# Kernel optimization log

Measured on AMD Instinct MI355X. Metric: run time of the kernel, lower is better.

The kernel has to match this reference:

```python
import jax, jax.numpy as jnp
import numpy as np

INPUT_DIM = 256
UNITS = 256
BATCH = 65536


def _glorot(key, shape):
    fan_in, fan_out = shape
    limit = np.sqrt(6.0 / (fan_in + fan_out)).astype(np.float32)
    return jax.random.uniform(key, shape, jnp.float32, -limit, limit)


def setup_inputs() -> dict:
    key = jax.random.key(0)
    ks = jax.random.split(key, 8)
    d = {
        "inputs": jax.random.normal(ks[0], (BATCH, INPUT_DIM), jnp.float32),
        "h_prev": jax.random.normal(ks[1], (BATCH, UNITS), jnp.float32),
        "c_prev": jax.random.normal(ks[2], (BATCH, UNITS), jnp.float32),
        "W_f": _glorot(ks[3], (INPUT_DIM + UNITS, UNITS)),
        "W_i": _glorot(ks[4], (INPUT_DIM + UNITS, UNITS)),
        "W_c": _glorot(ks[5], (INPUT_DIM + UNITS, UNITS)),
        "W_o": _glorot(ks[6], (INPUT_DIM + UNITS, UNITS)),
        "b_f": jnp.zeros((UNITS,), jnp.float32),
        "b_i": jnp.zeros((UNITS,), jnp.float32),
        "b_c": jnp.zeros((UNITS,), jnp.float32),
        "b_o": jnp.zeros((UNITS,), jnp.float32),
    }
    return d


def reference(inputs, h_prev, c_prev, W_f, W_i, W_c, W_o, b_f, b_i, b_c, b_o):
    # z: [B, input_dim + units]
    z = jnp.concatenate([inputs, h_prev], axis=-1)
    f = jax.nn.sigmoid(z @ W_f + b_f)
    i = jax.nn.sigmoid(z @ W_i + b_i)
    c_tilde = jnp.tanh(z @ W_c + b_c)
    c = f * c_prev + i * c_tilde
    o = jax.nn.sigmoid(z @ W_o + b_o)
    h = o * jnp.tanh(c)
    return h, c
```

## Files before the change

kernel.cpp:

```cpp
#include <hip/hip_runtime.h>
#include <stdint.h>

#define BATCH   65536
#define UNITS   256
#define KDIM    512
#define BM      64
#define BN      64
#define NCHUNK  8
#define GPAD    72
#define SMEM_BYTES 36864

using f32x16 = __attribute__((ext_vector_type(16))) float;
using bf16x8 = __attribute__((ext_vector_type(8))) short;

__device__ __forceinline__ short f2bf(float f) {
  union { float f; unsigned u; } v; v.f = f;
  unsigned r = v.u + 0x7FFFu + ((v.u >> 16) & 1u);
  return (short)(r >> 16);
}
__device__ __forceinline__ float bf2f(short s) {
  union { float f; unsigned u; } v; v.u = ((unsigned)(unsigned short)s) << 16;
  return v.f;
}

__global__ void cvt_weights(const float* __restrict__ Wf, const float* __restrict__ Wi,
                            const float* __restrict__ Wc, const float* __restrict__ Wo,
                            short* __restrict__ Wt) {
  int idx = blockIdx.x * 256 + threadIdx.x;
  int g   = idx >> 17;
  int k   = (idx >> 8) & 511;
  int col = idx & 255;
  const float* W = (g == 0) ? Wf : (g == 1) ? Wi : (g == 2) ? Wc : Wo;
  float val = W[k * 256 + col];
  int nb = col >> 6, n = col & 63;
  int c = k >> 6, kg = (k >> 3) & 7, k8 = k & 7;
  int out = ((((g * 4 + nb) * 8 + c) * 8 + kg) * 64 + n) * 8 + k8;
  Wt[out] = f2bf(val);
}

__global__ __launch_bounds__(256, 3) void lstm_fused(
    const float* __restrict__ x, const float* __restrict__ hprev,
    const float* __restrict__ cprev, const short* __restrict__ Wt,
    const float* __restrict__ bfp, const float* __restrict__ bip,
    const float* __restrict__ bcp, const float* __restrict__ bop,
    float* __restrict__ hout, float* __restrict__ cout)
{
  extern __shared__ __align__(16) char smem[];
  const int tid  = threadIdx.x;
  const int g    = tid >> 6;
  const int lane = tid & 63;
  const int la   = lane & 31;
  const int hh   = lane >> 5;

  int bid = blockIdx.x;
  int wg  = (bid & 7) * 512 + (bid >> 3);
  const int m0 = (wg >> 2) * BM;
  const int nb = wg & 3;
  const int n0 = nb * BN;

  const short* Bbase = Wt + ((size_t)(g * 4 + nb)) * 32768 + hh * 512 + la * 8;

  f32x16 acc[2][2] = {};

  const int arow = tid >> 2;
  const int q    = tid & 3;
  const int slotW = (arow ^ (q << 2)) & 63;

  auto ldA = [&](int c, float4* v) {
    const float* base = (c < 4) ? x : hprev;
    const float* rowp = base + (size_t)(m0 + arow) * 256 + (c & 3) * 64;
    v[0] = *(const float4*)(rowp + q * 8);
    v[1] = *(const float4*)(rowp + q * 8 + 4);
    v[2] = *(const float4*)(rowp + (q + 4) * 8);
    v[3] = *(const float4*)(rowp + (q + 4) * 8 + 4);
  };
  auto wrA = [&](int buf, const float4* v) {
    char* Ab = smem + buf * 8192;
#pragma unroll
    for (int j = 0; j < 2; ++j) {
      int kg = q + 4 * j;
      bf16x8 b;
      b[0] = f2bf(v[2*j].x); b[1] = f2bf(v[2*j].y);
      b[2] = f2bf(v[2*j].z); b[3] = f2bf(v[2*j].w);
      b[4] = f2bf(v[2*j+1].x); b[5] = f2bf(v[2*j+1].y);
      b[6] = f2bf(v[2*j+1].z); b[7] = f2bf(v[2*j+1].w);
      *(bf16x8*)(Ab + kg * 1024 + slotW * 16) = b;
    }
  };
  auto compute = [&](int c, int buf) {
    const char*  Ab = smem + buf * 8192;
    const short* Bc = Bbase + c * 4096;
#pragma unroll
    for (int ks = 0; ks < 4; ++ks) {
      const int kg   = 2 * ks + hh;
      const int slot = (la ^ ((kg & 3) << 2));
      const int off  = kg * 1024 + slot * 16;
      bf16x8 a0 = *(const bf16x8*)(Ab + off);
      bf16x8 a1 = *(const bf16x8*)(Ab + off + 512);
      bf16x8 b0 = *(const bf16x8*)(Bc + ks * 1024);
      bf16x8 b1 = *(const bf16x8*)(Bc + ks * 1024 + 256);
      acc[0][0] = __builtin_amdgcn_mfma_f32_32x32x16_bf16(a0, b0, acc[0][0], 0, 0, 0);
      acc[0][1] = __builtin_amdgcn_mfma_f32_32x32x16_bf16(a0, b1, acc[0][1], 0, 0, 0);
      acc[1][0] = __builtin_amdgcn_mfma_f32_32x32x16_bf16(a1, b0, acc[1][0], 0, 0, 0);
      acc[1][1] = __builtin_amdgcn_mfma_f32_32x32x16_bf16(a1, b1, acc[1][1], 0, 0, 0);
    }
  };

  {
    float4 v[4];
    ldA(0, v); wrA(0, v);
  }
  __syncthreads();
  int buf = 0;
  for (int c = 0; c < NCHUNK; ++c) {
    float4 nv[4];
    if (c + 1 < NCHUNK) ldA(c + 1, nv);
    compute(c, buf);
    if (c + 1 < NCHUNK) wrA(buf ^ 1, nv);
    __syncthreads();
    buf ^= 1;
  }

  const float* bptr = (g == 0) ? bfp : (g == 1) ? bip : (g == 2) ? bcp : bop;
  const float bias0 = bptr[n0 + la];
  const float bias1 = bptr[n0 + 32 + la];
  short* G = (short*)smem;
#pragma unroll
  for (int mi = 0; mi < 2; ++mi)
#pragma unroll
    for (int ni = 0; ni < 2; ++ni) {
      const float bias = ni ? bias1 : bias0;
#pragma unroll
      for (int r = 0; r < 16; ++r) {
        int row = (r & 3) + 8 * (r >> 2) + 4 * hh + mi * 32;
        int col = la + ni * 32;
        float v = acc[mi][ni][r] + bias;
        float a;
        if (g == 2) a = 1.f - 2.f / (__expf(2.f * v) + 1.f);
        else        a = 1.f / (1.f + __expf(-v));
        G[(g * 64 + row) * GPAD + col] = f2bf(a);
      }
    }
  __syncthreads();

  {
    const int vrow = tid >> 2;
    const int cq   = tid & 3;
    const size_t gi = (size_t)(m0 + vrow) * 256 + n0 + cq * 16;
    float4 cp[4];
#pragma unroll
    for (int i = 0; i < 4; ++i) cp[i] = *(const float4*)(cprev + gi + i * 4);

    bf16x8 gf[4][2];
#pragma unroll
    for (int gg = 0; gg < 4; ++gg) {
      const short* Gr = G + (gg * 64 + vrow) * GPAD + cq * 16;
      gf[gg][0] = *(const bf16x8*)(Gr);
      gf[gg][1] = *(const bf16x8*)(Gr + 8);
    }
    float ho[16], co[16];
#pragma unroll
    for (int e = 0; e < 16; ++e) {
      float fg = bf2f(gf[0][e >> 3][e & 7]);
      float ig = bf2f(gf[1][e >> 3][e & 7]);
      float cg = bf2f(gf[2][e >> 3][e & 7]);
      float og = bf2f(gf[3][e >> 3][e & 7]);
      float cpv = ((const float*)cp)[e];
      float cnew = fg * cpv + ig * cg;
      float hnew = og * (1.f - 2.f / (__expf(2.f * cnew) + 1.f));
      co[e] = cnew; ho[e] = hnew;
    }
#pragma unroll
    for (int i = 0; i < 4; ++i) {
      *(float4*)(hout + gi + i * 4) = ((const float4*)ho)[i];
      *(float4*)(cout + gi + i * 4) = ((const float4*)co)[i];
    }
  }
}

extern "C" void kernel_launch(void* const* d_in, const int* in_sizes, int n_in,
                              void* d_out, int out_size, void* d_ws, size_t ws_size,
                              hipStream_t stream) {
  const float* x     = (const float*)d_in[0];
  const float* hprev = (const float*)d_in[1];
  const float* cprev = (const float*)d_in[2];
  const float* Wf    = (const float*)d_in[3];
  const float* Wi    = (const float*)d_in[4];
  const float* Wc    = (const float*)d_in[5];
  const float* Wo    = (const float*)d_in[6];
  const float* bfp   = (const float*)d_in[7];
  const float* bip   = (const float*)d_in[8];
  const float* bcp   = (const float*)d_in[9];
  const float* bop   = (const float*)d_in[10];
  float* out = (float*)d_out;
  short* Wt  = (short*)d_ws;

  cvt_weights<<<2048, 256, 0, stream>>>(Wf, Wi, Wc, Wo, Wt);

  lstm_fused<<<dim3(4096), dim3(256), SMEM_BYTES, stream>>>(
      x, hprev, cprev, Wt, bfp, bip, bcp, bop,
      out, out + (size_t)BATCH * UNITS);
}
```

Before: 160.8 us.

## Prefetch B fragments into registers, deepen A pipeline, transpose gate staging

Weight (B) fragments are now prefetched into registers one chunk ahead, interleaved with the MFMAs. Activation (A) global loads run two chunks ahead so the LDS write happens before compute. The fp32-to-bf16 conversion uses packed hardware intrinsics, and barriers become a bare s_barrier after an LDS waitcnt. The gate staging layout is transposed to column-major with packed 8-byte writes. As a result the epilogue reads and writes c_prev, h and c with scalar strided accesses instead of float4 rows, which may cost global memory efficiency and raises register pressure.

```diff
diff --git a/kernel.cpp b/kernel.cpp
--- a/kernel.cpp
+++ b/kernel.cpp
@@ -1,13 +1,12 @@
 #include <hip/hip_runtime.h>
+#include <hip/hip_bf16.h>
 #include <stdint.h>
 
 #define BATCH   65536
 #define UNITS   256
-#define KDIM    512
-#define BM      64
-#define BN      64
 #define NCHUNK  8
-#define GPAD    72
+#define ROWP    72
+#define GSZ     (64 * ROWP)
 #define SMEM_BYTES 36864
 
 using f32x16 = __attribute__((ext_vector_type(16))) float;
@@ -22,6 +21,20 @@
   union { float f; unsigned u; } v; v.u = ((unsigned)(unsigned short)s) << 16;
   return v.f;
 }
+__device__ __forceinline__ unsigned pk2(float a, float b) {
+  union { __hip_bfloat162 h; unsigned u; } cv;
+  cv.h = __float22bfloat162_rn(make_float2(a, b));
+  return cv.u;
+}
+__device__ __forceinline__ bf16x8 cvt8(float4 a, float4 b) {
+  union { unsigned u[4]; bf16x8 v; } r;
+  r.u[0] = pk2(a.x, a.y); r.u[1] = pk2(a.z, a.w);
+  r.u[2] = pk2(b.x, b.y); r.u[3] = pk2(b.z, b.w);
+  return r.v;
+}
+
+#define BAR() do { asm volatile("s_waitcnt lgkmcnt(0)" ::: "memory"); \
+                   __builtin_amdgcn_s_barrier(); } while (0)
 
 __global__ void cvt_weights(const float* __restrict__ Wf, const float* __restrict__ Wi,
                             const float* __restrict__ Wc, const float* __restrict__ Wo,
@@ -54,16 +67,17 @@
 
   int bid = blockIdx.x;
   int wg  = (bid & 7) * 512 + (bid >> 3);
-  const int m0 = (wg >> 2) * BM;
+  const int m0 = (wg >> 2) * 64;
   const int nb = wg & 3;
-  const int n0 = nb * BN;
+  const int n0 = nb * 64;
 
   const short* Bbase = Wt + ((size_t)(g * 4 + nb)) * 32768 + hh * 512 + la * 8;
 
   f32x16 acc[2][2] = {};
-
-  const int arow = tid >> 2;
-  const int q    = tid & 3;
+  bf16x8 breg[8];
+
+  const int arow  = tid >> 2;
+  const int q     = tid & 3;
   const int slotW = (arow ^ (q << 2)) & 63;
 
   auto ldA = [&](int c, float4* v) {
@@ -76,48 +90,43 @@
   };
   auto wrA = [&](int buf, const float4* v) {
     char* Ab = smem + buf * 8192;
-#pragma unroll
-    for (int j = 0; j < 2; ++j) {
-      int kg = q + 4 * j;
-      bf16x8 b;
-      b[0] = f2bf(v[2*j].x); b[1] = f2bf(v[2*j].y);
-      b[2] = f2bf(v[2*j].z); b[3] = f2bf(v[2*j].w);
-      b[4] = f2bf(v[2*j+1].x); b[5] = f2bf(v[2*j+1].y);
-      b[6] = f2bf(v[2*j+1].z); b[7] = f2bf(v[2*j+1].w);
-      *(bf16x8*)(Ab + kg * 1024 + slotW * 16) = b;
-    }
+    *(bf16x8*)(Ab + q * 1024 + slotW * 16)       = cvt8(v[0], v[1]);
+    *(bf16x8*)(Ab + (q + 4) * 1024 + slotW * 16) = cvt8(v[2], v[3]);
   };
-  auto compute = [&](int c, int buf) {
+  auto loadB = [&](int c, int ks) {
+    const short* Bc = Bbase + (size_t)c * 4096 + ks * 1024;
+    breg[2 * ks]     = *(const bf16x8*)(Bc);
+    breg[2 * ks + 1] = *(const bf16x8*)(Bc + 256);
+  };
+
+  float4 v[4];
+  ldA(0, v); wrA(0, v);
+  ldA(1, v);
+#pragma unroll
+  for (int ks = 0; ks < 4; ++ks) loadB(0, ks);
+  BAR();
+
+  int buf = 0;
+  for (int c = 0; c < NCHUNK; ++c) {
+    if (c + 1 < NCHUNK) wrA(buf ^ 1, v);
+    if (c + 2 < NCHUNK) ldA(c + 2, v);
     const char*  Ab = smem + buf * 8192;
-    const short* Bc = Bbase + c * 4096;
+    const short* Bn = Bbase + (size_t)((c + 1) & 7) * 4096;
 #pragma unroll
     for (int ks = 0; ks < 4; ++ks) {
       const int kg   = 2 * ks + hh;
-      const int slot = (la ^ ((kg & 3) << 2));
+      const int slot = la ^ ((kg & 3) << 2);
       const int off  = kg * 1024 + slot * 16;
       bf16x8 a0 = *(const bf16x8*)(Ab + off);
       bf16x8 a1 = *(const bf16x8*)(Ab + off + 512);
-      bf16x8 b0 = *(const bf16x8*)(Bc + ks * 1024);
-      bf16x8 b1 = *(const bf16x8*)(Bc + ks * 1024 + 256);
-      acc[0][0] = __builtin_amdgcn_mfma_f32_32x32x16_bf16(a0, b0, acc[0][0], 0, 0, 0);
-      acc[0][1] = __builtin_amdgcn_mfma_f32_32x32x16_bf16(a0, b1, acc[0][1], 0, 0, 0);
-      acc[1][0] = __builtin_amdgcn_mfma_f32_32x32x16_bf16(a1, b0, acc[1][0], 0, 0, 0);
-      acc[1][1] = __builtin_amdgcn_mfma_f32_32x32x16_bf16(a1, b1, acc[1][1], 0, 0, 0);
-    }
-  };
-
-  {
-    float4 v[4];
-    ldA(0, v); wrA(0, v);
-  }
-  __syncthreads();
-  int buf = 0;
-  for (int c = 0; c < NCHUNK; ++c) {
-    float4 nv[4];
-    if (c + 1 < NCHUNK) ldA(c + 1, nv);
-    compute(c, buf);
-    if (c + 1 < NCHUNK) wrA(buf ^ 1, nv);
-    __syncthreads();
+      acc[0][0] = __builtin_amdgcn_mfma_f32_32x32x16_bf16(a0, breg[2*ks],   acc[0][0], 0, 0, 0);
+      acc[0][1] = __builtin_amdgcn_mfma_f32_32x32x16_bf16(a0, breg[2*ks+1], acc[0][1], 0, 0, 0);
+      acc[1][0] = __builtin_amdgcn_mfma_f32_32x32x16_bf16(a1, breg[2*ks],   acc[1][0], 0, 0, 0);
+      acc[1][1] = __builtin_amdgcn_mfma_f32_32x32x16_bf16(a1, breg[2*ks+1], acc[1][1], 0, 0, 0);
+      breg[2*ks]     = *(const bf16x8*)(Bn + ks * 1024);
+      breg[2*ks + 1] = *(const bf16x8*)(Bn + ks * 1024 + 256);
+    }
+    BAR();
     buf ^= 1;
   }
 
@@ -130,50 +139,47 @@
 #pragma unroll
     for (int ni = 0; ni < 2; ++ni) {
       const float bias = ni ? bias1 : bias0;
-#pragma unroll
-      for (int r = 0; r < 16; ++r) {
-        int row = (r & 3) + 8 * (r >> 2) + 4 * hh + mi * 32;
-        int col = la + ni * 32;
-        float v = acc[mi][ni][r] + bias;
-        float a;
-        if (g == 2) a = 1.f - 2.f / (__expf(2.f * v) + 1.f);
-        else        a = 1.f / (1.f + __expf(-v));
-        G[(g * 64 + row) * GPAD + col] = f2bf(a);
+      const int   col  = la + ni * 32;
+#pragma unroll
+      for (int rq = 0; rq < 4; ++rq) {
+        const int row0 = rq * 8 + 4 * hh + mi * 32;
+        float t[4];
+#pragma unroll
+        for (int e = 0; e < 4; ++e) {
+          float vv = acc[mi][ni][rq * 4 + e] + bias;
+          t[e] = (g == 2) ? (1.f - 2.f / (__expf(2.f * vv) + 1.f))
+                          : (1.f / (1.f + __expf(-vv)));
+        }
+        uint2 u; u.x = pk2(t[0], t[1]); u.y = pk2(t[2], t[3]);
+        *(uint2*)(G + g * GSZ + col * ROWP + row0) = u;
       }
     }
-  __syncthreads();
+  BAR();
 
   {
-    const int vrow = tid >> 2;
-    const int cq   = tid & 3;
-    const size_t gi = (size_t)(m0 + vrow) * 256 + n0 + cq * 16;
-    float4 cp[4];
-#pragma unroll
-    for (int i = 0; i < 4; ++i) cp[i] = *(const float4*)(cprev + gi + i * 4);
-
+    const int col = tid & 63;
+    const int rg  = tid >> 6;
+    const short* Gp = G + col * ROWP + rg * 16;
     bf16x8 gf[4][2];
 #pragma unroll
     for (int gg = 0; gg < 4; ++gg) {
-      const short* Gr = G + (gg * 64 + vrow) * GPAD + cq * 16;
-      gf[gg][0] = *(const bf16x8*)(Gr);
-      gf[gg][1] = *(const bf16x8*)(Gr + 8);
-    }
-    float ho[16], co[16];
-#pragma unroll
-    for (int e = 0; e < 16; ++e) {
-      float fg = bf2f(gf[0][e >> 3][e & 7]);
-      float ig = bf2f(gf[1][e >> 3][e & 7]);
-      float cg = bf2f(gf[2][e >> 3][e & 7]);
-      float og = bf2f(gf[3][e >> 3][e & 7]);
-      float cpv = ((const float*)cp)[e];
-      float cnew = fg * cpv + ig * cg;
+      gf[gg][0] = *(const bf16x8*)(Gp + gg * GSZ);
+      gf[gg][1] = *(const bf16x8*)(Gp + gg * GSZ + 8);
+    }
+    const size_t gbase = (size_t)(m0 + rg * 16) * 256 + n0 + col;
+    float cp[16];
+#pragma unroll
+    for (int j = 0; j < 16; ++j) cp[j] = cprev[gbase + (size_t)j * 256];
+#pragma unroll
+    for (int j = 0; j < 16; ++j) {
+      float fg = bf2f(gf[0][j >> 3][j & 7]);
+      float ig = bf2f(gf[1][j >> 3][j & 7]);
+      float cg = bf2f(gf[2][j >> 3][j & 7]);
+      float og = bf2f(gf[3][j >> 3][j & 7]);
+      float cnew = fg * cp[j] + ig * cg;
       float hnew = og * (1.f - 2.f / (__expf(2.f * cnew) + 1.f));
-      co[e] = cnew; ho[e] = hnew;
-    }
-#pragma unroll
-    for (int i = 0; i < 4; ++i) {
-      *(float4*)(hout + gi + i * 4) = ((const float4*)ho)[i];
-      *(float4*)(cout + gi + i * 4) = ((const float4*)co)[i];
+      hout[gbase + (size_t)j * 256] = hnew;
+      cout[gbase + (size_t)j * 256] = cnew;
     }
   }
 }
```

Result: faster. 149.2 us (-7.2%).
